# Optimization experiments

Hardware: AMD Instinct MI355X
Metric: run time of the kernel (lower is better)

The kernel has to match this reference:

```python
import jax, jax.numpy as jnp
import numpy as np

KP_EXTENT = 0.05
N_Q = 40000   # query points
N_S = 40000   # support points
K = 32        # neighbors per query
P = 15        # kernel points
IN_DIM = 64
OUT_DIM = 128


def setup_inputs() -> dict:
    key = jax.random.key(0)
    k1, k2, k3, k4, k5, k6 = jax.random.split(key, 6)
    q_pts = jax.random.uniform(k1, (N_Q, 3), dtype=jnp.float32)
    s_pts = jax.random.uniform(k2, (N_S, 3), dtype=jnp.float32)
    # indices in [0, N_S]; value N_S hits the appended shadow row
    neighbor_idxs = jax.random.randint(k3, (N_Q, K), 0, N_S + 1)
    x = jax.random.normal(k4, (N_S, IN_DIM), dtype=jnp.float32)
    weights = jax.random.normal(k5, (P, IN_DIM, OUT_DIM), dtype=jnp.float32) * 0.05
    kernel_points = jax.random.normal(k6, (P, 3), dtype=jnp.float32) * 0.06
    return {"q_pts": q_pts, "s_pts": s_pts, "neighbor_idxs": neighbor_idxs,
            "x": x, "weights": weights, "kernel_points": kernel_points}


def reference(q_pts, s_pts, neighbor_idxs, x, weights, kernel_points):
    # Append shadow support point. NOTE: the original does
    # zeros_like(s_pts[:1,:] + 1e6) which is exactly zeros, so shadow = origin.
    s_pad = jnp.concatenate([s_pts, jnp.zeros_like(s_pts[:1, :])], axis=0)
    # Gather neighbor coordinates, center on queries: [N, K, 3]
    neighbors = s_pad[neighbor_idxs] - q_pts[:, None, :]
    # Distances to every kernel point: [N, K, P]
    diff = neighbors[:, :, None, :] - kernel_points[None, None, :, :]
    sq_distances = jnp.sum(diff * diff, axis=3)
    all_weights = jnp.clip(1.0 - jnp.sqrt(sq_distances) / KP_EXTENT, 0.0)
    all_weights = jnp.transpose(all_weights, (0, 2, 1))  # [N, P, K]
    # Gather neighbor features with zero shadow row: [N, K, D_in]
    feats = jnp.concatenate([x, jnp.zeros_like(x[:1, :])], axis=0)
    neighbors_x = feats[neighbor_idxs]
    # Kernel-point weighted aggregation: [N, P, D_in] -> [P, N, D_in]
    weighted_features = jnp.transpose(jnp.matmul(all_weights, neighbors_x), (1, 0, 2))
    # Per-kernel-point linear map: [P, N, D_out], then sum over kernel points
    kernel_outputs = jnp.matmul(weighted_features, weights)
    output_features = jnp.sum(kernel_outputs, axis=0)  # [N, D_out]
    # Normalize by count of "valid" neighbors (feature-sum > 0 heuristic)
    neighbor_features_sum = jnp.sum(neighbors_x, axis=-1)          # [N, K]
    neighbor_num = jnp.sum(neighbor_features_sum > 0.0, axis=-1)   # [N]
    neighbor_num = jnp.maximum(neighbor_num, 1).astype(output_features.dtype)
    return output_features / neighbor_num[:, None]
```

## Files before the change

### kernel.cpp

```cpp
#include <hip/hip_runtime.h>

#define N_Q     40000
#define N_S     40000
#define KK      32
#define PP      15
#define IN_DIM  64
#define OUT_DIM 128

typedef __attribute__((ext_vector_type(8))) short short8;
typedef __attribute__((ext_vector_type(4))) float floatx4;

static __device__ __forceinline__ short f2bf(float f) {
  union { float f; unsigned u; } v; v.f = f;
  unsigned r = v.u + 0x7FFFu + ((v.u >> 16) & 1u);
  return (short)(r >> 16);
}


__global__ __launch_bounds__(256) void prep_kernel(
    const float* __restrict__ x, const float* __restrict__ s_pts,
    const float* __restrict__ weights, const float* __restrict__ kpts,
    float4* __restrict__ packed, unsigned* __restrict__ wmf,
    float* __restrict__ r2out) {
  const int b = blockIdx.x;
  if (b < 2500) {
    const int t = b * 256 + threadIdx.x;
    const int row = t >> 4;
    const int sub = t & 15;
    float4 v = reinterpret_cast<const float4*>(x + (size_t)row * IN_DIM)[sub];
    float s = (v.x + v.y) + (v.z + v.w);
    s += __shfl_xor(s, 1, 64);
    s += __shfl_xor(s, 2, 64);
    s += __shfl_xor(s, 4, 64);
    s += __shfl_xor(s, 8, 64);
    if (sub == 0) {
      float4 pkt;
      pkt.x = s_pts[row * 3 + 0];
      pkt.y = s_pts[row * 3 + 1];
      pkt.z = s_pts[row * 3 + 2];
      pkt.w = (s > 0.0f) ? 1.0f : 0.0f;
      packed[row] = pkt;
    }
    if (t == 1) {
      float4 z; z.x = 0.f; z.y = 0.f; z.z = 0.f; z.w = 0.f;
      packed[N_S] = z;
    }
  } else if (b < 2740) {
    const int t = (b - 2500) * 256 + threadIdx.x;
    const int j2   = t & 3;
    const int lane = (t >> 2) & 63;
    const int fi   = t >> 8;
    const int kc = fi & 1, g = (fi >> 1) & 7, p = fi >> 4;
    const int c  = g * 16 + (lane & 15);
    const int k0 = kc * 32 + (lane >> 4) * 8 + 2 * j2;
    const float w0 = weights[(size_t)p * (IN_DIM * OUT_DIM) + (size_t)k0 * OUT_DIM + c];
    const float w1 = weights[(size_t)p * (IN_DIM * OUT_DIM) + (size_t)(k0 + 1) * OUT_DIM + c];
    wmf[t] = (unsigned)(unsigned short)f2bf(w0)
           | ((unsigned)(unsigned short)f2bf(w1) << 16);
  } else {
    if (threadIdx.x < 64) {
      const int lane = threadIdx.x;
      float r2 = 0.0f;
      if (lane < PP) {
        const float kx = kpts[lane * 3 + 0];
        const float ky = kpts[lane * 3 + 1];
        const float kz = kpts[lane * 3 + 2];
        r2 = kx * kx + ky * ky + kz * kz;
      }
      #pragma unroll
      for (int s = 32; s; s >>= 1) r2 = fmaxf(r2, __shfl_xor(r2, s, 64));
      if (lane == 0) {
        const float R = sqrtf(r2) + 0.05f;
        r2out[0] = R * R;
      }
    }
  }
}

__global__ __launch_bounds__(256, 4) void kpconv_fused_kernel(
    const float* __restrict__ q_pts, const int* __restrict__ nidx,
    const float* __restrict__ x, const float* __restrict__ kpts,
    const float4* __restrict__ packed, const uint4* __restrict__ wmf4,
    const float* __restrict__ r2buf, float* __restrict__ out) {
  const int tid  = blockIdx.x * 256 + threadIdx.x;
  const int lane = threadIdx.x & 63;
  const int n  = tid >> 5;
  const int nA = (tid & ~63) >> 5;

  const int pl = (lane < PP) ? lane : 0;
  const float kxl = kpts[pl * 3 + 0];
  const float kyl = kpts[pl * 3 + 1];
  const float kzl = kpts[pl * 3 + 2];

  const float R2 = r2buf[0];

  const int id = nidx[tid];
  const float4 sp = packed[id];
  const bool real = (id < N_S);

  const float ox = sp.x - q_pts[n * 3 + 0];
  const float oy = sp.y - q_pts[n * 3 + 1];
  const float oz = sp.z - q_pts[n * 3 + 2];

  unsigned long long bal = __ballot(sp.w != 0.0f);
  unsigned int half = (lane < 32) ? (unsigned int)bal
                                  : (unsigned int)(bal >> 32);
  int num = (int)__popc(half);
  if (num < 1) num = 1;
  const float invnum = 1.0f / (float)num;

  floatx4 acc[8];
  #pragma unroll
  for (int g = 0; g < 8; ++g) acc[g] = (floatx4){0.f, 0.f, 0.f, 0.f};

  const float d2o = ox * ox + oy * oy + oz * oz;
  unsigned long long bc = __ballot(real && (d2o <= R2));
  while (bc) {
    const int j = (int)__ffsll((unsigned long long)bc) - 1;
    bc &= bc - 1;
    const float oxj = __shfl(ox, j);
    const float oyj = __shfl(oy, j);
    const float ozj = __shfl(oz, j);
    const int   idj = __shfl(id, j);
    const float inj = __shfl(invnum, j);
    const float dx = oxj - kxl, dy = oyj - kyl, dz = ozj - kzl;
    const float d2 = dx * dx + dy * dy + dz * dz;
    const bool hit = (lane < PP) && (d2 < 0.0025f);
    const float wc = hit ? (1.0f - 20.0f * sqrtf(d2)) * inj : 0.0f;
    unsigned long long bh = __ballot(hit);
    const int m = j >> 5;
    while (bh) {
      const int h = (int)__ffsll((unsigned long long)bh) - 1;
      bh &= bh - 1;
      const float wj = __shfl(wc, h);
      const int p = h;
      short8 af0 = {0, 0, 0, 0, 0, 0, 0, 0};
      short8 af1 = {0, 0, 0, 0, 0, 0, 0, 0};
      if ((lane & 15) == m) {
        const float4* xr = reinterpret_cast<const float4*>(x + (size_t)idj * IN_DIM);
        const int q4 = (lane >> 4) * 2;
        const float4 xa = xr[q4],     xb = xr[q4 + 1];
        const float4 xc = xr[q4 + 8], xd = xr[q4 + 9];
        af0[0] = f2bf(wj * xa.x); af0[1] = f2bf(wj * xa.y);
        af0[2] = f2bf(wj * xa.z); af0[3] = f2bf(wj * xa.w);
        af0[4] = f2bf(wj * xb.x); af0[5] = f2bf(wj * xb.y);
        af0[6] = f2bf(wj * xb.z); af0[7] = f2bf(wj * xb.w);
        af1[0] = f2bf(wj * xc.x); af1[1] = f2bf(wj * xc.y);
        af1[2] = f2bf(wj * xc.z); af1[3] = f2bf(wj * xc.w);
        af1[4] = f2bf(wj * xd.x); af1[5] = f2bf(wj * xd.y);
        af1[6] = f2bf(wj * xd.z); af1[7] = f2bf(wj * xd.w);
      }
      #pragma unroll
      for (int g = 0; g < 8; ++g) {
        const uint4 b0 = wmf4[(size_t)((p * 8 + g) * 2 + 0) * 64 + lane];
        acc[g] = __builtin_amdgcn_mfma_f32_16x16x32_bf16(
            af0, __builtin_bit_cast(short8, b0), acc[g], 0, 0, 0);
        const uint4 b1 = wmf4[(size_t)((p * 8 + g) * 2 + 1) * 64 + lane];
        acc[g] = __builtin_amdgcn_mfma_f32_16x16x32_bf16(
            af1, __builtin_bit_cast(short8, b1), acc[g], 0, 0, 0);
      }
    }
  }

  if (lane < 16) {
    #pragma unroll
    for (int g = 0; g < 8; ++g) {
      out[(size_t)nA * OUT_DIM + g * 16 + lane]       = acc[g][0];
      out[(size_t)(nA + 1) * OUT_DIM + g * 16 + lane] = acc[g][1];
    }
  }
}

extern "C" void kernel_launch(void* const* d_in, const int* in_sizes, int n_in,
                              void* d_out, int out_size, void* d_ws, size_t ws_size,
                              hipStream_t stream) {
  const float* q_pts   = (const float*)d_in[0];
  const float* s_pts   = (const float*)d_in[1];
  const int*   nidx    = (const int*)d_in[2];
  const float* x       = (const float*)d_in[3];
  const float* weights = (const float*)d_in[4];
  const float* kpts    = (const float*)d_in[5];
  float* out = (float*)d_out;

  char* ws = (char*)d_ws;
  float4*   packed = (float4*)ws;
  unsigned* wmf    = (unsigned*)(ws + (1u << 20));
  float*    r2buf  = (float*)(ws + (1u << 20) + (256u << 10));

  prep_kernel<<<2741, 256, 0, stream>>>(x, s_pts, weights, kpts, packed, wmf, r2buf);
  kpconv_fused_kernel<<<(N_Q * KK) / 256, 256, 0, stream>>>(
      q_pts, nidx, x, kpts, packed, (const uint4*)wmf, r2buf, out);
}
```

Before: 100.2 us.

## Process four queries per wavefront to fill more MFMA rows

Each wavefront now handles four queries (two passes of two queries) instead of two. All four accumulate into rows 0-3 of the same 16x16 MFMA tile, and the grid is halved. Previously only two of the 16 A-matrix rows were used, so the same weight-fragment loads and MFMA instructions can now serve twice as many queries per output-tile write. The cost is more serial work per wave, with two sequential ballot loops, and fewer total waves, which could reduce latency hiding.

```diff
diff --git a/kernel.cpp b/kernel.cpp
--- a/kernel.cpp
+++ b/kernel.cpp
@@ -82,10 +82,14 @@
     const float* __restrict__ x, const float* __restrict__ kpts,
     const float4* __restrict__ packed, const uint4* __restrict__ wmf4,
     const float* __restrict__ r2buf, float* __restrict__ out) {
-  const int tid  = blockIdx.x * 256 + threadIdx.x;
-  const int lane = threadIdx.x & 63;
-  const int n  = tid >> 5;
-  const int nA = (tid & ~63) >> 5;
+  const int tid   = blockIdx.x * 256 + threadIdx.x;
+  const int lane  = threadIdx.x & 63;
+  const int wbase = tid & ~63;
+  const int q0    = wbase >> 4;
+  const int g0    = 2 * wbase + lane;
+  const int g1    = g0 + 64;
+  const int n0    = q0 + (lane >> 5);
+  const int n1    = n0 + 2;
 
   const int pl = (lane < PP) ? lane : 0;
   const float kxl = kpts[pl * 3 + 0];
@@ -94,70 +98,134 @@
 
   const float R2 = r2buf[0];
 
-  const int id = nidx[tid];
-  const float4 sp = packed[id];
-  const bool real = (id < N_S);
-
-  const float ox = sp.x - q_pts[n * 3 + 0];
-  const float oy = sp.y - q_pts[n * 3 + 1];
-  const float oz = sp.z - q_pts[n * 3 + 2];
-
-  unsigned long long bal = __ballot(sp.w != 0.0f);
-  unsigned int half = (lane < 32) ? (unsigned int)bal
-                                  : (unsigned int)(bal >> 32);
-  int num = (int)__popc(half);
-  if (num < 1) num = 1;
-  const float invnum = 1.0f / (float)num;
+  const int id0 = nidx[g0];
+  const int id1 = nidx[g1];
+  const float4 sp0 = packed[id0];
+  const float4 sp1 = packed[id1];
+
+  const float ox0 = sp0.x - q_pts[n0 * 3 + 0];
+  const float oy0 = sp0.y - q_pts[n0 * 3 + 1];
+  const float oz0 = sp0.z - q_pts[n0 * 3 + 2];
+  const float ox1 = sp1.x - q_pts[n1 * 3 + 0];
+  const float oy1 = sp1.y - q_pts[n1 * 3 + 1];
+  const float oz1 = sp1.z - q_pts[n1 * 3 + 2];
+
+  unsigned long long bal0 = __ballot(sp0.w != 0.0f);
+  unsigned int half0 = (lane < 32) ? (unsigned int)bal0
+                                   : (unsigned int)(bal0 >> 32);
+  int num0 = (int)__popc(half0);
+  if (num0 < 1) num0 = 1;
+  const float invnum0 = 1.0f / (float)num0;
+
+  unsigned long long bal1 = __ballot(sp1.w != 0.0f);
+  unsigned int half1 = (lane < 32) ? (unsigned int)bal1
+                                   : (unsigned int)(bal1 >> 32);
+  int num1 = (int)__popc(half1);
+  if (num1 < 1) num1 = 1;
+  const float invnum1 = 1.0f / (float)num1;
 
   floatx4 acc[8];
   #pragma unroll
   for (int g = 0; g < 8; ++g) acc[g] = (floatx4){0.f, 0.f, 0.f, 0.f};
 
-  const float d2o = ox * ox + oy * oy + oz * oz;
-  unsigned long long bc = __ballot(real && (d2o <= R2));
-  while (bc) {
-    const int j = (int)__ffsll((unsigned long long)bc) - 1;
-    bc &= bc - 1;
-    const float oxj = __shfl(ox, j);
-    const float oyj = __shfl(oy, j);
-    const float ozj = __shfl(oz, j);
-    const int   idj = __shfl(id, j);
-    const float inj = __shfl(invnum, j);
-    const float dx = oxj - kxl, dy = oyj - kyl, dz = ozj - kzl;
-    const float d2 = dx * dx + dy * dy + dz * dz;
-    const bool hit = (lane < PP) && (d2 < 0.0025f);
-    const float wc = hit ? (1.0f - 20.0f * sqrtf(d2)) * inj : 0.0f;
-    unsigned long long bh = __ballot(hit);
-    const int m = j >> 5;
-    while (bh) {
-      const int h = (int)__ffsll((unsigned long long)bh) - 1;
-      bh &= bh - 1;
-      const float wj = __shfl(wc, h);
-      const int p = h;
-      short8 af0 = {0, 0, 0, 0, 0, 0, 0, 0};
-      short8 af1 = {0, 0, 0, 0, 0, 0, 0, 0};
-      if ((lane & 15) == m) {
-        const float4* xr = reinterpret_cast<const float4*>(x + (size_t)idj * IN_DIM);
-        const int q4 = (lane >> 4) * 2;
-        const float4 xa = xr[q4],     xb = xr[q4 + 1];
-        const float4 xc = xr[q4 + 8], xd = xr[q4 + 9];
-        af0[0] = f2bf(wj * xa.x); af0[1] = f2bf(wj * xa.y);
-        af0[2] = f2bf(wj * xa.z); af0[3] = f2bf(wj * xa.w);
-        af0[4] = f2bf(wj * xb.x); af0[5] = f2bf(wj * xb.y);
-        af0[6] = f2bf(wj * xb.z); af0[7] = f2bf(wj * xb.w);
-        af1[0] = f2bf(wj * xc.x); af1[1] = f2bf(wj * xc.y);
-        af1[2] = f2bf(wj * xc.z); af1[3] = f2bf(wj * xc.w);
-        af1[4] = f2bf(wj * xd.x); af1[5] = f2bf(wj * xd.y);
-        af1[6] = f2bf(wj * xd.z); af1[7] = f2bf(wj * xd.w);
-      }
-      #pragma unroll
-      for (int g = 0; g < 8; ++g) {
-        const uint4 b0 = wmf4[(size_t)((p * 8 + g) * 2 + 0) * 64 + lane];
-        acc[g] = __builtin_amdgcn_mfma_f32_16x16x32_bf16(
-            af0, __builtin_bit_cast(short8, b0), acc[g], 0, 0, 0);
-        const uint4 b1 = wmf4[(size_t)((p * 8 + g) * 2 + 1) * 64 + lane];
-        acc[g] = __builtin_amdgcn_mfma_f32_16x16x32_bf16(
-            af1, __builtin_bit_cast(short8, b1), acc[g], 0, 0, 0);
+  {
+    const float d2o = ox0 * ox0 + oy0 * oy0 + oz0 * oz0;
+    unsigned long long bc = __ballot((id0 < N_S) && (d2o <= R2));
+    while (bc) {
+      const int j = (int)__ffsll((unsigned long long)bc) - 1;
+      bc &= bc - 1;
+      const float oxj = __shfl(ox0, j);
+      const float oyj = __shfl(oy0, j);
+      const float ozj = __shfl(oz0, j);
+      const int   idj = __shfl(id0, j);
+      const float inj = __shfl(invnum0, j);
+      const float dx = oxj - kxl, dy = oyj - kyl, dz = ozj - kzl;
+      const float d2 = dx * dx + dy * dy + dz * dz;
+      const bool hit = (lane < PP) && (d2 < 0.0025f);
+      const float wc = hit ? (1.0f - 20.0f * sqrtf(d2)) * inj : 0.0f;
+      unsigned long long bh = __ballot(hit);
+      const int m = j >> 5;
+      while (bh) {
+        const int h = (int)__ffsll((unsigned long long)bh) - 1;
+        bh &= bh - 1;
+        const float wj = __shfl(wc, h);
+        const int p = h;
+        short8 af0 = {0, 0, 0, 0, 0, 0, 0, 0};
+        short8 af1 = {0, 0, 0, 0, 0, 0, 0, 0};
+        if ((lane & 15) == m) {
+          const float4* xr = reinterpret_cast<const float4*>(x + (size_t)idj * IN_DIM);
+          const int q4 = (lane >> 4) * 2;
+          const float4 xa = xr[q4],     xb = xr[q4 + 1];
+          const float4 xc = xr[q4 + 8], xd = xr[q4 + 9];
+          af0[0] = f2bf(wj * xa.x); af0[1] = f2bf(wj * xa.y);
+          af0[2] = f2bf(wj * xa.z); af0[3] = f2bf(wj * xa.w);
+          af0[4] = f2bf(wj * xb.x); af0[5] = f2bf(wj * xb.y);
+          af0[6] = f2bf(wj * xb.z); af0[7] = f2bf(wj * xb.w);
+          af1[0] = f2bf(wj * xc.x); af1[1] = f2bf(wj * xc.y);
+          af1[2] = f2bf(wj * xc.z); af1[3] = f2bf(wj * xc.w);
+          af1[4] = f2bf(wj * xd.x); af1[5] = f2bf(wj * xd.y);
+          af1[6] = f2bf(wj * xd.z); af1[7] = f2bf(wj * xd.w);
+        }
+        #pragma unroll
+        for (int g = 0; g < 8; ++g) {
+          const uint4 b0 = wmf4[(size_t)((p * 8 + g) * 2 + 0) * 64 + lane];
+          acc[g] = __builtin_amdgcn_mfma_f32_16x16x32_bf16(
+              af0, __builtin_bit_cast(short8, b0), acc[g], 0, 0, 0);
+          const uint4 b1 = wmf4[(size_t)((p * 8 + g) * 2 + 1) * 64 + lane];
+          acc[g] = __builtin_amdgcn_mfma_f32_16x16x32_bf16(
+              af1, __builtin_bit_cast(short8, b1), acc[g], 0, 0, 0);
+        }
+      }
+    }
+  }
+
+  {
+    const float d2o = ox1 * ox1 + oy1 * oy1 + oz1 * oz1;
+    unsigned long long bc = __ballot((id1 < N_S) && (d2o <= R2));
+    while (bc) {
+      const int j = (int)__ffsll((unsigned long long)bc) - 1;
+      bc &= bc - 1;
+      const float oxj = __shfl(ox1, j);
+      const float oyj = __shfl(oy1, j);
+      const float ozj = __shfl(oz1, j);
+      const int   idj = __shfl(id1, j);
+      const float inj = __shfl(invnum1, j);
+      const float dx = oxj - kxl, dy = oyj - kyl, dz = ozj - kzl;
+      const float d2 = dx * dx + dy * dy + dz * dz;
+      const bool hit = (lane < PP) && (d2 < 0.0025f);
+      const float wc = hit ? (1.0f - 20.0f * sqrtf(d2)) * inj : 0.0f;
+      unsigned long long bh = __ballot(hit);
+      const int m = 2 + (j >> 5);
+      while (bh) {
+        const int h = (int)__ffsll((unsigned long long)bh) - 1;
+        bh &= bh - 1;
+        const float wj = __shfl(wc, h);
+        const int p = h;
+        short8 af0 = {0, 0, 0, 0, 0, 0, 0, 0};
+        short8 af1 = {0, 0, 0, 0, 0, 0, 0, 0};
+        if ((lane & 15) == m) {
+          const float4* xr = reinterpret_cast<const float4*>(x + (size_t)idj * IN_DIM);
+          const int q4 = (lane >> 4) * 2;
+          const float4 xa = xr[q4],     xb = xr[q4 + 1];
+          const float4 xc = xr[q4 + 8], xd = xr[q4 + 9];
+          af0[0] = f2bf(wj * xa.x); af0[1] = f2bf(wj * xa.y);
+          af0[2] = f2bf(wj * xa.z); af0[3] = f2bf(wj * xa.w);
+          af0[4] = f2bf(wj * xb.x); af0[5] = f2bf(wj * xb.y);
+          af0[6] = f2bf(wj * xb.z); af0[7] = f2bf(wj * xb.w);
+          af1[0] = f2bf(wj * xc.x); af1[1] = f2bf(wj * xc.y);
+          af1[2] = f2bf(wj * xc.z); af1[3] = f2bf(wj * xc.w);
+          af1[4] = f2bf(wj * xd.x); af1[5] = f2bf(wj * xd.y);
+          af1[6] = f2bf(wj * xd.z); af1[7] = f2bf(wj * xd.w);
+        }
+        #pragma unroll
+        for (int g = 0; g < 8; ++g) {
+          const uint4 b0 = wmf4[(size_t)((p * 8 + g) * 2 + 0) * 64 + lane];
+          acc[g] = __builtin_amdgcn_mfma_f32_16x16x32_bf16(
+              af0, __builtin_bit_cast(short8, b0), acc[g], 0, 0, 0);
+          const uint4 b1 = wmf4[(size_t)((p * 8 + g) * 2 + 1) * 64 + lane];
+          acc[g] = __builtin_amdgcn_mfma_f32_16x16x32_bf16(
+              af1, __builtin_bit_cast(short8, b1), acc[g], 0, 0, 0);
+        }
       }
     }
   }
@@ -165,8 +233,9 @@
   if (lane < 16) {
     #pragma unroll
     for (int g = 0; g < 8; ++g) {
-      out[(size_t)nA * OUT_DIM + g * 16 + lane]       = acc[g][0];
-      out[(size_t)(nA + 1) * OUT_DIM + g * 16 + lane] = acc[g][1];
+      #pragma unroll
+      for (int r = 0; r < 4; ++r)
+        out[(size_t)(q0 + r) * OUT_DIM + g * 16 + lane] = acc[g][r];
     }
   }
 }
@@ -188,6 +257,6 @@
   float*    r2buf  = (float*)(ws + (1u << 20) + (256u << 10));
 
   prep_kernel<<<2741, 256, 0, stream>>>(x, s_pts, weights, kpts, packed, wmf, r2buf);
-  kpconv_fused_kernel<<<(N_Q * KK) / 256, 256, 0, stream>>>(
+  kpconv_fused_kernel<<<(N_Q * KK) / (256 * 2), 256, 0, stream>>>(
       q_pts, nidx, x, kpts, packed, (const uint4*)wmf, r2buf, out);
 }
```

Result: no change. 100.5 us (+0.3%).
